# Optimization experiments

Measured on AMD Instinct MI355X. Metric: run time of the kernel, lower is better.

Reference implementation:

```python
import jax, jax.numpy as jnp
import numpy as np

DIM = 1536; NH = 12; HD = 128; C2 = HD // 2          # rope half-dim = 64
F, H, W = 1, 30, 52
FRAME = H * W                                         # 1560 tokens/frame
SINK_FRAMES = 1; LOCAL_ATTN = 6
SINK = SINK_FRAMES * FRAME                            # 1560
MAX_ATTN = LOCAL_ATTN * 1560                          # 9360
CACHE = 9360                                          # kv cache length
GLOBAL_END = 9360; LOCAL_END_CACHE = 9360             # cache state before step
SPLITS = (C2 - 2 * (C2 // 3), C2 // 3, C2 // 3)       # (22, 21, 21)
EPS = 1e-6


def setup_inputs() -> dict:
    key = jax.random.key(0)
    ks = jax.random.split(key, 12)
    s = F * H * W
    rn = lambda k, sh, sc=1.0: jax.random.normal(k, sh, jnp.float32) * sc
    x = rn(ks[0], (1, s, DIM))
    Wq = rn(ks[1], (DIM, DIM), 0.02); Wk = rn(ks[2], (DIM, DIM), 0.02)
    Wv = rn(ks[3], (DIM, DIM), 0.02); Wo = rn(ks[4], (DIM, DIM), 0.02)
    zb = jnp.zeros((DIM,), jnp.float32)
    angles = jax.random.uniform(ks[5], (1024, C2), jnp.float32) * (2.0 * np.pi)
    freqs_cos = jnp.cos(angles); freqs_sin = jnp.sin(angles)
    cache_k = rn(ks[6], (1, CACHE, NH, HD)); cache_v = rn(ks[7], (1, CACHE, NH, HD))
    return dict(x=x, Wq=Wq, bq=zb, Wk=Wk, bk=zb, Wv=Wv, bv=zb, Wo=Wo, bo=zb,
                nq_w=jnp.ones((DIM,), jnp.float32), nk_w=jnp.ones((DIM,), jnp.float32),
                cache_k=cache_k, cache_v=cache_v,
                freqs_cos=freqs_cos, freqs_sin=freqs_sin,
                seq_lens=jnp.array([s], jnp.int32),
                grid_sizes=jnp.array([[F, H, W]], jnp.int32),
                current_start=GLOBAL_END)


def _rmsnorm(x, w):
    return x * jax.lax.rsqrt(jnp.mean(x * x, -1, keepdims=True) + EPS) * w


def _grid_table(table, start_frame):
    """table [1024, C2] -> per-token rope factors [S, 1, C2] over the (F,H,W) grid."""
    s0, s1, s2 = SPLITS
    tf, th, tw = table[:, :s0], table[:, s0:s0 + s1], table[:, s0 + s1:]
    fp = jnp.broadcast_to(tf[start_frame:start_frame + F][:, None, None, :], (F, H, W, s0))
    hp = jnp.broadcast_to(th[:H][None, :, None, :], (F, H, W, s1))
    wp = jnp.broadcast_to(tw[:W][None, None, :, :], (F, H, W, s2))
    return jnp.concatenate([fp, hp, wp], -1).reshape(F * H * W, 1, C2)


def _rope(x, cos, sin):
    # x: [b, s, n, d]; cos/sin: [s, 1, C2] (complex multiply in real arithmetic)
    b, s, n, d = x.shape
    xp = x.reshape(b, s, n, d // 2, 2)
    xr, xi = xp[..., 0], xp[..., 1]
    c, sn = cos[None], sin[None]                      # [1, s, 1, C2]
    out_r = xr * c - xi * sn
    out_i = xr * sn + xi * c
    return jnp.stack([out_r, out_i], -1).reshape(b, s, n, d)


def reference(x, Wq, bq, Wk, bk, Wv, bv, Wo, bo, nq_w, nk_w,
              cache_k, cache_v, freqs_cos, freqs_sin,
              seq_lens, grid_sizes, current_start):
    b, s = x.shape[:2]
    q = _rmsnorm(x @ Wq.T + bq, nq_w).reshape(b, s, NH, HD)
    k = _rmsnorm(x @ Wk.T + bk, nk_w).reshape(b, s, NH, HD)
    v = (x @ Wv.T + bv).reshape(b, s, NH, HD)

    start_frame = int(current_start) // FRAME
    cos = _grid_table(freqs_cos, start_frame)
    sin = _grid_table(freqs_sin, start_frame)
    rq = _rope(q, cos, sin)
    rk = _rope(k, cos, sin)

    # --- static cache bookkeeping (roll_and_insert path; all Python ints) ---
    num_new = s
    current_end = int(current_start) + num_new
    num_evicted = num_new + LOCAL_END_CACHE - CACHE           # 1560
    num_rolled = LOCAL_END_CACHE - num_evicted - SINK         # 6240
    local_end = LOCAL_END_CACHE + current_end - GLOBAL_END - num_evicted  # 9360
    local_start = local_end - num_new                         # 7800 == SINK + num_rolled
    temp_k = jnp.concatenate(
        [cache_k[:, :SINK], cache_k[:, SINK + num_evicted:SINK + num_evicted + num_rolled], rk], axis=1)
    temp_v = jnp.concatenate(
        [cache_v[:, :SINK], cache_v[:, SINK + num_evicted:SINK + num_evicted + num_rolled], v], axis=1)

    # --- sink + sliding-window attention ---
    local_budget = MAX_ATTN - SINK
    win_start = max(SINK, local_end - local_budget)
    k_cat = jnp.concatenate([temp_k[:, :SINK], temp_k[:, win_start:local_end]], axis=1)
    v_cat = jnp.concatenate([temp_v[:, :SINK], temp_v[:, win_start:local_end]], axis=1)

    logits = jnp.einsum('bqhd,bkhd->bhqk', rq, k_cat) * (HD ** -0.5)
    probs = jax.nn.softmax(logits, axis=-1)
    out = jnp.einsum('bhqk,bkhd->bqhd', probs, v_cat)
    y = out.reshape(b, s, DIM) @ Wo.T + bo
    return y
```

## Files before the change

kernel.cpp:

```cpp
#include <hip/hip_runtime.h>
#include <hip/hip_bf16.h>

typedef __bf16 bf16;
typedef __bf16 bf16x2 __attribute__((ext_vector_type(2)));
typedef __bf16 bf16x4 __attribute__((ext_vector_type(4)));
typedef __bf16 bf16x8 __attribute__((ext_vector_type(8)));
typedef float f32x4 __attribute__((ext_vector_type(4)));
typedef float f32x16 __attribute__((ext_vector_type(16)));
typedef unsigned u32x2 __attribute__((ext_vector_type(2)));

#define DIM 1536
#define NH 12
#define HD 128
#define SEQ 1560
#define KV 9360
#define KVP 9408
#define SINK 1560
#define NEWBASE 7800
#define QSCALE_L2E (0.08838834764831845f * 1.4426950408889634f)
#define NSPLIT 3
#define CHUNK 3136
#define NT 98
#define KB 32
#define QBLK 128
#define NQT 13

__device__ __forceinline__ void gl_lds16(const void* g, void* l) {
  __builtin_amdgcn_global_load_lds(
      (const __attribute__((address_space(1))) unsigned int*)g,
      (__attribute__((address_space(3))) unsigned int*)l, 16, 0, 0);
}

__device__ __forceinline__ f32x16 mfma32(bf16x8 a, bf16x8 b, f32x16 c) {
  return __builtin_amdgcn_mfma_f32_32x32x16_bf16(a, b, c, 0, 0, 0);
}

struct CastBatch {
  const float* src[5];
  bf16* dst[5];
  int n[5];
};
__global__ __launch_bounds__(256) void castall(CastBatch cb) {
  const float* src = cb.src[blockIdx.y];
  bf16* dst = cb.dst[blockIdx.y];
  int n = cb.n[blockIdx.y];
  int i = (blockIdx.x * 256 + threadIdx.x) * 8;
  if (i < n) {
    float4 a = *(const float4*)(src + i);
    float4 b = *(const float4*)(src + i + 4);
    bf16x8 o;
    o[0] = (bf16)a.x; o[1] = (bf16)a.y; o[2] = (bf16)a.z; o[3] = (bf16)a.w;
    o[4] = (bf16)b.x; o[5] = (bf16)b.y; o[6] = (bf16)b.z; o[7] = (bf16)b.w;
    *(bf16x8*)(dst + i) = o;
  }
}

__global__ __launch_bounds__(256) void clear_pad(bf16* __restrict__ Kcat,
                                                 bf16* __restrict__ Vt) {
  int h = blockIdx.y;
  int i = blockIdx.x * 256 + threadIdx.x;
  if (i < (KVP - KV) * HD) {
    int r = KV + i / HD, d = i % HD;
    Kcat[((size_t)h * KVP + r) * HD + d] = (bf16)0.f;
    int dv = i / (KVP - KV), j = KV + i % (KVP - KV);
    Vt[((size_t)h * HD + dv) * KVP + j] = (bf16)0.f;
  }
}

struct GemmBatch {
  const bf16* B[3];
  const float* bias[3];
  float* C[3];
};

#define BM 128
#define BN 128
#define BK 32

__global__ __launch_bounds__(256, 2) void gemm_bt(const bf16* __restrict__ A,
                                                  GemmBatch gb, int M) {
  const bf16* Bw = gb.B[blockIdx.z];
  const float* bias = gb.bias[blockIdx.z];
  float* C = gb.C[blockIdx.z];
  int bm = blockIdx.x * BM;
  int bn = blockIdx.y * BN;

  __shared__ bf16 Alds[2][BM][BK];
  __shared__ bf16 Blds[2][BN][BK];

  int t = threadIdx.x;
  int lane = t & 63;
  int wave = t >> 6;
  int wr = wave >> 1, wc = wave & 1;
  int fr = lane & 15;
  int fo = (lane >> 4) * 8;

  f32x4 acc[4][4] = {};

  const int NK = DIM / BK;
  int colA = (lane & 3) * 8;
  int lrow = lane >> 2;

#define STAGEG(buf, k0)                                                     \
  {                                                                         \
    _Pragma("unroll") for (int p = 0; p < 2; ++p) {                         \
      int rbase = wave * 16 + p * 64;                                       \
      int ga = bm + rbase + lrow;                                           \
      if (ga > M - 1) ga = M - 1;                                           \
      gl_lds16(A + (size_t)ga * DIM + (k0) + colA, &Alds[buf][rbase][0]);   \
      int gbv = bn + rbase + lrow;                                          \
      gl_lds16(Bw + (size_t)gbv * DIM + (k0) + colA, &Blds[buf][rbase][0]); \
    }                                                                       \
  }

  STAGEG(0, 0);
  int cur = 0;
  for (int ks = 0; ks < NK; ++ks) {
    __syncthreads();
    if (ks + 1 < NK) STAGEG(cur ^ 1, (ks + 1) * BK);
    bf16x8 af[4], bfv[4];
#pragma unroll
    for (int i = 0; i < 4; ++i)
      af[i] = *(const bf16x8*)&Alds[cur][wr * 64 + i * 16 + fr][fo];
#pragma unroll
    for (int j = 0; j < 4; ++j)
      bfv[j] = *(const bf16x8*)&Blds[cur][wc * 64 + j * 16 + fr][fo];
#pragma unroll
    for (int i = 0; i < 4; ++i)
#pragma unroll
      for (int j = 0; j < 4; ++j)
        acc[i][j] = __builtin_amdgcn_mfma_f32_16x16x32_bf16(af[i], bfv[j],
                                                            acc[i][j], 0, 0, 0);
    cur ^= 1;
  }
#undef STAGEG

  int g4 = (lane >> 4) * 4;
#pragma unroll
  for (int i = 0; i < 4; ++i) {
    int mbase = bm + wr * 64 + i * 16 + g4;
#pragma unroll
    for (int j = 0; j < 4; ++j) {
      int col = bn + wc * 64 + j * 16 + fr;
      float bv = bias[col];
#pragma unroll
      for (int r = 0; r < 4; ++r) {
        int m = mbase + r;
        if (m < M) C[(size_t)m * DIM + col] = acc[i][j][r] + bv;
      }
    }
  }
}

__global__ __launch_bounds__(256) void norm_rope(
    const float* __restrict__ qraw, const float* __restrict__ kraw,
    const float* __restrict__ nqw, const float* __restrict__ nkw,
    const float* __restrict__ fcos, const float* __restrict__ fsin,
    bf16* __restrict__ Qh, bf16* __restrict__ Kcat) {
  int tok = blockIdx.x;
  int tid = threadIdx.x;
  const float* qr = qraw + (size_t)tok * DIM;
  const float* kr = kraw + (size_t)tok * DIM;
  float sq = 0.f, sk = 0.f;
  for (int c = tid; c < DIM; c += 256) {
    float a = qr[c];
    sq += a * a;
    float b = kr[c];
    sk += b * b;
  }
#pragma unroll
  for (int off = 32; off; off >>= 1) {
    sq += __shfl_down(sq, off);
    sk += __shfl_down(sk, off);
  }
  __shared__ float red[2][4];
  int w = tid >> 6;
  if ((tid & 63) == 0) {
    red[0][w] = sq;
    red[1][w] = sk;
  }
  __syncthreads();
  sq = red[0][0] + red[0][1] + red[0][2] + red[0][3];
  sk = red[1][0] + red[1][1] + red[1][2] + red[1][3];
  float rsq = rsqrtf(sq * (1.0f / DIM) + 1e-6f);
  float rsk = rsqrtf(sk * (1.0f / DIM) + 1e-6f);

  int hrow = tok / 52, wrow = tok % 52;
  for (int p = tid; p < NH * 64; p += 256) {
    int n = p >> 6, i = p & 63;
    int trow = (i < 22) ? 6 : (i < 43 ? hrow : wrow);
    float cs = fcos[trow * 64 + i];
    float sn = fsin[trow * 64 + i];
    int c = n * HD + 2 * i;
    float xr = qr[c] * rsq * nqw[c];
    float xi = qr[c + 1] * rsq * nqw[c + 1];
    bf16x2 qo;
    qo[0] = (bf16)((xr * cs - xi * sn) * QSCALE_L2E);
    qo[1] = (bf16)((xr * sn + xi * cs) * QSCALE_L2E);
    *(bf16x2*)(Qh + ((size_t)n * SEQ + tok) * HD + 2 * i) = qo;
    float yr = kr[c] * rsk * nkw[c];
    float yi = kr[c + 1] * rsk * nkw[c + 1];
    bf16x2 ko;
    ko[0] = (bf16)(yr * cs - yi * sn);
    ko[1] = (bf16)(yr * sn + yi * cs);
    *(bf16x2*)(Kcat + ((size_t)n * KVP + NEWBASE + tok) * HD + 2 * i) = ko;
  }
}

__global__ __launch_bounds__(256) void build_kcat(const float* __restrict__ cache_k,
                                                  bf16* __restrict__ Kcat) {
  int j = blockIdx.x;
  int src = j < SINK ? j : j + SINK;
  const float* sp = cache_k + (size_t)src * DIM;
  for (int c4 = threadIdx.x; c4 < DIM / 4; c4 += 256) {
    float4 v = *(const float4*)(sp + c4 * 4);
    int c = c4 * 4;
    int n = c >> 7, d = c & 127;
    bf16x4 o;
    o[0] = (bf16)v.x; o[1] = (bf16)v.y; o[2] = (bf16)v.z; o[3] = (bf16)v.w;
    *(bf16x4*)(Kcat + ((size_t)n * KVP + j) * HD + d) = o;
  }
}

__global__ __launch_bounds__(256) void build_vt(const float* __restrict__ cache_v,
                                                const float* __restrict__ vraw,
                                                bf16* __restrict__ Vt) {
  int h = blockIdx.y;
  int j0 = blockIdx.x * 64;
  __shared__ bf16 T[128][72];
  int tid = threadIdx.x;
  for (int idx = tid; idx < 64 * 32; idx += 256) {
    int jl = idx >> 5, s = idx & 31;
    int j = j0 + jl;
    if (j >= KV) continue;
    const float* sp;
    if (j < NEWBASE) {
      int srcj = j < SINK ? j : j + SINK;
      sp = cache_v + (size_t)srcj * DIM + h * HD;
    } else {
      sp = vraw + (size_t)(j - NEWBASE) * DIM + h * HD;
    }
    float4 v = *(const float4*)(sp + s * 4);
    T[s * 4 + 0][jl] = (bf16)v.x;
    T[s * 4 + 1][jl] = (bf16)v.y;
    T[s * 4 + 2][jl] = (bf16)v.z;
    T[s * 4 + 3][jl] = (bf16)v.w;
  }
  __syncthreads();
  for (int idx = tid; idx < 128 * 16; idx += 256) {
    int d = idx >> 4, g = idx & 15;
    int j = j0 + g * 4;
    if (j + 4 > KV) continue;
    bf16x4 o;
    o[0] = T[d][4 * g];
    o[1] = T[d][4 * g + 1];
    o[2] = T[d][4 * g + 2];
    o[3] = T[d][4 * g + 3];
    *(bf16x4*)(Vt + ((size_t)h * HD + d) * KVP + j) = o;
  }
}

__global__ __launch_bounds__(256, 2) void attn_split(const bf16* __restrict__ Qh,
                                                     const bf16* __restrict__ Kcat,
                                                     const bf16* __restrict__ Vtg,
                                                     float* __restrict__ Opart,
                                                     float* __restrict__ MLpart) {
  int orig = blockIdx.x;
  int xcd = orig & 7, jj = orig >> 3;
  int wgid = (xcd < 4 ? xcd * 59 : 236 + (xcd - 4) * 58) + jj;
  int qt = wgid % NQT;
  int h = (wgid / NQT) % NH;
  int sp = wgid / (NQT * NH);
  int q0 = qt * QBLK;
  int c0 = sp * CHUNK;

  int t = threadIdx.x, lane = t & 63, w = t >> 6;
  int ql = lane & 31, hi = lane >> 5;

  __shared__ __align__(16) bf16 Vlds[2][128 * KB];

  int qrow = q0 + w * 32 + ql;
  int qcl = qrow < SEQ ? qrow : SEQ - 1;
  const bf16* Qp = Qh + ((size_t)h * SEQ + qcl) * HD + hi * 8;
  bf16x8 qreg[8];
#pragma unroll
  for (int ks = 0; ks < 8; ++ks) qreg[ks] = *(const bf16x8*)(Qp + ks * 16);

  int vadd[2];
#pragma unroll
  for (int p = 0; p < 2; ++p) {
    int m = (2 * w + p) * 64 + lane;
    int dV = m >> 2, cV = m & 3;
    vadd[p] = dV * KVP + (cV ^ ((dV >> 1) & 3)) * 8;
  }

  int voff[4][2];
#pragma unroll
  for (int db = 0; db < 4; ++db)
#pragma unroll
    for (int ks = 0; ks < 2; ++ks)
      voff[db][ks] = (db * 32 + ql) * 64 + (((ks * 2 + hi) ^ ((ql >> 1) & 3)) * 16);

  const bf16* Vhp = Vtg + (size_t)h * HD * KVP;
  const bf16* Kl0 = Kcat + (size_t)h * KVP * HD + (size_t)(c0 + ql) * HD + hi * 8;

  f32x16 oacc[4] = {};
  float m_q = -1e38f, l_q = 0.f;

#define STAGEV(buf, j0v)                                                      \
  {                                                                           \
    const bf16* Vs = Vhp + (j0v);                                             \
    _Pragma("unroll") for (int p = 0; p < 2; ++p)                             \
        gl_lds16(Vs + vadd[p], (char*)&Vlds[buf][0] + w * 2048 + p * 1024);   \
  }

#define KLOAD(KR, TI)                                                         \
  {                                                                           \
    const bf16* Kl = Kl0 + (TI) * (KB * HD);                                  \
    _Pragma("unroll") for (int ks = 0; ks < 8; ++ks)                          \
        KR[ks] = *(const bf16x8*)(Kl + ks * 16);                              \
  }

#define TILE_BODY(KR, TI)                                                     \
  {                                                                           \
    int j0 = c0 + (TI)*KB;                                                    \
    const char* Vc = (const char*)&Vlds[cur][0];                              \
    f32x16 s0 = {};                                                           \
    __builtin_amdgcn_s_setprio(1);                                            \
    _Pragma("unroll") for (int ks = 0; ks < 8; ++ks)                          \
        s0 = mfma32(KR[ks], qreg[ks], s0);                                    \
    __builtin_amdgcn_s_setprio(0);                                            \
    if (j0 + KB > KV) {                                                       \
      _Pragma("unroll") for (int reg = 0; reg < 16; ++reg) {                  \
        int kk = (reg & 3) + 8 * (reg >> 2) + 4 * hi;                         \
        if (j0 + kk >= KV) s0[reg] = -1e38f;                                  \
      }                                                                       \
    }                                                                         \
    float m8[8];                                                              \
    _Pragma("unroll") for (int r = 0; r < 8; ++r)                             \
        m8[r] = fmaxf(s0[r], s0[r + 8]);                                      \
    float mx = fmaxf(fmaxf(fmaxf(m8[0], m8[4]), fmaxf(m8[1], m8[5])),         \
                     fmaxf(fmaxf(m8[2], m8[6]), fmaxf(m8[3], m8[7])));        \
    mx = fmaxf(mx, __shfl_xor(mx, 32));                                       \
    if (__any(mx - m_q > 8.f)) {                                              \
      float mnew = fmaxf(m_q, mx);                                            \
      float corr = exp2f(m_q - mnew);                                         \
      m_q = mnew;                                                             \
      l_q *= corr;                                                            \
      _Pragma("unroll") for (int reg = 0; reg < 16; ++reg) {                  \
        int qsrc = (reg & 3) + 8 * (reg >> 2) + 4 * hi;                       \
        float c = __shfl(corr, qsrc);                                         \
        _Pragma("unroll") for (int db = 0; db < 4; ++db) oacc[db][reg] *= c;  \
      }                                                                       \
    }                                                                         \
    _Pragma("unroll") for (int r = 0; r < 16; ++r)                            \
        s0[r] = exp2f(s0[r] - m_q);                                           \
    float t8[8];                                                              \
    _Pragma("unroll") for (int r = 0; r < 8; ++r) t8[r] = s0[r] + s0[r + 8];  \
    float sum = ((t8[0] + t8[4]) + (t8[1] + t8[5])) +                         \
                ((t8[2] + t8[6]) + (t8[3] + t8[7]));                          \
    sum += __shfl_xor(sum, 32);                                               \
    l_q += sum;                                                               \
    bf16x8 pa[2];                                                             \
    _Pragma("unroll") for (int ks = 0; ks < 2; ++ks) {                        \
      const int r0 = ks * 8;                                                  \
      bf16x2 p0, p1, p2, p3;                                                  \
      p0[0] = (bf16)s0[r0 + 0]; p0[1] = (bf16)s0[r0 + 1];                     \
      p1[0] = (bf16)s0[r0 + 2]; p1[1] = (bf16)s0[r0 + 3];                     \
      p2[0] = (bf16)s0[r0 + 4]; p2[1] = (bf16)s0[r0 + 5];                     \
      p3[0] = (bf16)s0[r0 + 6]; p3[1] = (bf16)s0[r0 + 7];                     \
      unsigned x0 = __builtin_bit_cast(unsigned, p0);                         \
      unsigned x1 = __builtin_bit_cast(unsigned, p1);                         \
      unsigned y0 = __builtin_bit_cast(unsigned, p2);                         \
      unsigned y1 = __builtin_bit_cast(unsigned, p3);                         \
      u32x2 r0v = __builtin_amdgcn_permlane32_swap(x0, y0, false, false);     \
      u32x2 r1v = __builtin_amdgcn_permlane32_swap(x1, y1, false, false);     \
      int4 tmp;                                                               \
      tmp.x = (int)r0v[0];                                                    \
      tmp.y = (int)r1v[0];                                                    \
      tmp.z = (int)r0v[1];                                                    \
      tmp.w = (int)r1v[1];                                                    \
      pa[ks] = __builtin_bit_cast(bf16x8, tmp);                               \
    }                                                                         \
    __builtin_amdgcn_s_setprio(1);                                            \
    _Pragma("unroll") for (int db = 0; db < 4; ++db)                          \
        _Pragma("unroll") for (int ks = 0; ks < 2; ++ks)                      \
            oacc[db] = mfma32(pa[ks], *(const bf16x8*)(Vc + voff[db][ks]),    \
                              oacc[db]);                                      \
    __builtin_amdgcn_s_setprio(0);                                            \
    __syncthreads();                                                          \
    cur ^= 1;                                                                 \
  }

  bf16x8 kA[8], kB[8];
  STAGEV(0, c0);
  KLOAD(kA, 0);
  __syncthreads();
  int cur = 0;

#pragma unroll 1
  for (int it = 0; it < NT / 2; ++it) {
    int ti = 2 * it;
    STAGEV(cur ^ 1, c0 + (ti + 1) * KB);
    KLOAD(kB, ti + 1);
    TILE_BODY(kA, ti);
    if (ti + 2 < NT) {
      STAGEV(cur ^ 1, c0 + (ti + 2) * KB);
      KLOAD(kA, ti + 2);
    }
    TILE_BODY(kB, ti + 1);
  }
#undef TILE_BODY
#undef KLOAD
#undef STAGEV

  float* Oh = Opart + ((size_t)sp * NH + h) * SEQ * HD;
  float* MLh = MLpart + ((size_t)sp * NH + h) * SEQ * 2;
#pragma unroll
  for (int reg = 0; reg < 16; ++reg) {
    int q = q0 + w * 32 + (reg & 3) + 8 * (reg >> 2) + 4 * hi;
    if (q >= SEQ) continue;
#pragma unroll
    for (int db = 0; db < 4; ++db)
      Oh[(size_t)q * HD + db * 32 + ql] = oacc[db][reg];
  }
  if (lane < 32) {
    int q = q0 + w * 32 + ql;
    if (q < SEQ) {
      MLh[q * 2 + 0] = m_q;
      MLh[q * 2 + 1] = l_q;
    }
  }
}

__global__ __launch_bounds__(256) void attn_merge(const float* __restrict__ Opart,
                                                  const float* __restrict__ MLpart,
                                                  bf16* __restrict__ Aout) {
  int idx = blockIdx.x * 2 + (threadIdx.x >> 7);
  if (idx >= NH * SEQ) return;
  int d = threadIdx.x & 127;
  int h = idx / SEQ, q = idx % SEQ;
  float m[NSPLIT];
  float M = -1e38f;
#pragma unroll
  for (int s = 0; s < NSPLIT; ++s) {
    m[s] = MLpart[(((size_t)s * NH + h) * SEQ + q) * 2];
    M = fmaxf(M, m[s]);
  }
  float L = 0.f, o = 0.f;
#pragma unroll
  for (int s = 0; s < NSPLIT; ++s) {
    float wgt = exp2f(m[s] - M);
    L += MLpart[(((size_t)s * NH + h) * SEQ + q) * 2 + 1] * wgt;
    o += Opart[((((size_t)s * NH + h) * SEQ + q)) * HD + d] * wgt;
  }
  Aout[(size_t)q * DIM + h * HD + d] = (bf16)(o / L);
}

extern "C" void kernel_launch(void* const* d_in, const int* in_sizes, int n_in,
                              void* d_out, int out_size, void* d_ws, size_t ws_size,
                              hipStream_t stream) {
  const float* x = (const float*)d_in[0];
  const float* Wq = (const float*)d_in[1];
  const float* bq = (const float*)d_in[2];
  const float* Wk = (const float*)d_in[3];
  const float* bk = (const float*)d_in[4];
  const float* Wv = (const float*)d_in[5];
  const float* bv = (const float*)d_in[6];
  const float* Wo = (const float*)d_in[7];
  const float* bo = (const float*)d_in[8];
  const float* nqw = (const float*)d_in[9];
  const float* nkw = (const float*)d_in[10];
  const float* cache_k = (const float*)d_in[11];
  const float* cache_v = (const float*)d_in[12];
  const float* fcos = (const float*)d_in[13];
  const float* fsin = (const float*)d_in[14];
  float* out = (float*)d_out;

  char* ws = (char*)d_ws;
  size_t off = 0;
  auto alloc = [&](size_t bytes) {
    char* p = ws + off;
    off += (bytes + 255) & ~(size_t)255;
    return p;
  };
  const int XN = SEQ * DIM;
  const int WN = DIM * DIM;
  bf16* xb = (bf16*)alloc((size_t)XN * 2);
  bf16* Wqb = (bf16*)alloc((size_t)WN * 2);
  bf16* Wkb = (bf16*)alloc((size_t)WN * 2);
  bf16* Wvb = (bf16*)alloc((size_t)WN * 2);
  bf16* Wob = (bf16*)alloc((size_t)WN * 2);
  bf16* QhB = (bf16*)alloc((size_t)NH * SEQ * HD * 2);
  bf16* Kcat = (bf16*)alloc((size_t)NH * KVP * HD * 2);
  bf16* Vt = (bf16*)alloc((size_t)NH * HD * KVP * 2);
  bf16* Aout = (bf16*)alloc((size_t)XN * 2);
  float* MLpart = (float*)alloc((size_t)NSPLIT * NH * SEQ * 2 * 4);
  float* Opart = (float*)alloc((size_t)NSPLIT * NH * SEQ * HD * 4);
  float* qraw = Opart;
  float* kraw = qraw + XN;
  float* vraw = kraw + XN;

  CastBatch cb;
  cb.src[0] = x;  cb.dst[0] = xb;  cb.n[0] = XN;
  cb.src[1] = Wq; cb.dst[1] = Wqb; cb.n[1] = WN;
  cb.src[2] = Wk; cb.dst[2] = Wkb; cb.n[2] = WN;
  cb.src[3] = Wv; cb.dst[3] = Wvb; cb.n[3] = WN;
  cb.src[4] = Wo; cb.dst[4] = Wob; cb.n[4] = WN;
  castall<<<dim3((XN + 2047) / 2048, 5), 256, 0, stream>>>(cb);

  clear_pad<<<dim3(((KVP - KV) * HD + 255) / 256, NH), 256, 0, stream>>>(Kcat, Vt);

  GemmBatch gqkv;
  gqkv.B[0] = Wqb; gqkv.B[1] = Wkb; gqkv.B[2] = Wvb;
  gqkv.bias[0] = bq; gqkv.bias[1] = bk; gqkv.bias[2] = bv;
  gqkv.C[0] = qraw; gqkv.C[1] = kraw; gqkv.C[2] = vraw;
  gemm_bt<<<dim3(13, 12, 3), 256, 0, stream>>>(xb, gqkv, SEQ);

  norm_rope<<<SEQ, 256, 0, stream>>>(qraw, kraw, nqw, nkw, fcos, fsin, QhB, Kcat);
  build_kcat<<<NEWBASE, 256, 0, stream>>>(cache_k, Kcat);
  build_vt<<<dim3(147, NH), 256, 0, stream>>>(cache_v, vraw, Vt);

  attn_split<<<dim3(NQT * NH * NSPLIT), 256, 0, stream>>>(QhB, Kcat, Vt, Opart, MLpart);
  attn_merge<<<(NH * SEQ + 1) / 2, 256, 0, stream>>>(Opart, MLpart, Aout);

  GemmBatch gout;
  gout.B[0] = Wob; gout.B[1] = Wob; gout.B[2] = Wob;
  gout.bias[0] = bo; gout.bias[1] = bo; gout.bias[2] = bo;
  gout.C[0] = out; gout.C[1] = out; gout.C[2] = out;
  gemm_bt<<<dim3(13, 12, 1), 256, 0, stream>>>(Aout, gout, SEQ);
}
```

Measured before the change: 352.2 us.

## Stage K through LDS and software-pipeline QK^T one tile ahead of softmax-PV

K tiles are now staged into swizzled LDS with async global-to-LDS copies, replacing direct per-lane register loads. V gets a triple buffer. The loop is restructured so QK^T for tile i runs alongside softmax and PV for tile i-1, letting the MFMA work of the two stages interleave with the exp/reduction work. This costs more LDS (two K buffers plus three V buffers per block) and extra LDS reads for K, which may reduce occupancy or add bank traffic.

```diff
diff --git a/kernel.cpp b/kernel.cpp
--- a/kernel.cpp
+++ b/kernel.cpp
@@ -277,7 +277,8 @@
   int t = threadIdx.x, lane = t & 63, w = t >> 6;
   int ql = lane & 31, hi = lane >> 5;
 
-  __shared__ __align__(16) bf16 Vlds[2][128 * KB];
+  __shared__ __align__(16) bf16 Klds[2][KB * 128];
+  __shared__ __align__(16) bf16 Vlds[3][128 * KB];
 
   int qrow = q0 + w * 32 + ql;
   int qcl = qrow < SEQ ? qrow : SEQ - 1;
@@ -286,14 +287,20 @@
 #pragma unroll
   for (int ks = 0; ks < 8; ++ks) qreg[ks] = *(const bf16x8*)(Qp + ks * 16);
 
-  int vadd[2];
+  int kadd[2], vadd[2];
 #pragma unroll
   for (int p = 0; p < 2; ++p) {
     int m = (2 * w + p) * 64 + lane;
+    int rK = m >> 4, cK = m & 15;
+    kadd[p] = rK * HD + (cK ^ (rK & 15)) * 8;
     int dV = m >> 2, cV = m & 3;
     vadd[p] = dV * KVP + (cV ^ ((dV >> 1) & 3)) * 8;
   }
 
+  int koff[8];
+#pragma unroll
+  for (int ks = 0; ks < 8; ++ks)
+    koff[ks] = ql * 256 + (((ks * 2 + hi) ^ (ql & 15)) * 16);
   int voff[4][2];
 #pragma unroll
   for (int db = 0; db < 4; ++db)
@@ -301,44 +308,52 @@
     for (int ks = 0; ks < 2; ++ks)
       voff[db][ks] = (db * 32 + ql) * 64 + (((ks * 2 + hi) ^ ((ql >> 1) & 3)) * 16);
 
+  const bf16* Khp = Kcat + (size_t)h * KVP * HD;
   const bf16* Vhp = Vtg + (size_t)h * HD * KVP;
-  const bf16* Kl0 = Kcat + (size_t)h * KVP * HD + (size_t)(c0 + ql) * HD + hi * 8;
+  char* Kb = (char*)&Klds[0][0];
+  char* Vb = (char*)&Vlds[0][0];
 
   f32x16 oacc[4] = {};
   float m_q = -1e38f, l_q = 0.f;
-
-#define STAGEV(buf, j0v)                                                      \
+  f32x16 sA, sB;
+  int vst, vpv;
+
+#define STAGEK(kbuf, TIs)                                                     \
   {                                                                           \
-    const bf16* Vs = Vhp + (j0v);                                             \
+    const bf16* Ks = Khp + (size_t)(c0 + (TIs)*KB) * HD;                      \
     _Pragma("unroll") for (int p = 0; p < 2; ++p)                             \
-        gl_lds16(Vs + vadd[p], (char*)&Vlds[buf][0] + w * 2048 + p * 1024);   \
-  }
-
-#define KLOAD(KR, TI)                                                         \
+        gl_lds16(Ks + kadd[p], Kb + (kbuf)*8192 + w * 2048 + p * 1024);       \
+  }
+#define STAGEV(vbuf, TIs)                                                     \
   {                                                                           \
-    const bf16* Kl = Kl0 + (TI) * (KB * HD);                                  \
-    _Pragma("unroll") for (int ks = 0; ks < 8; ++ks)                          \
-        KR[ks] = *(const bf16x8*)(Kl + ks * 16);                              \
-  }
-
-#define TILE_BODY(KR, TI)                                                     \
+    const bf16* Vs = Vhp + (c0 + (TIs)*KB);                                   \
+    _Pragma("unroll") for (int p = 0; p < 2; ++p)                             \
+        gl_lds16(Vs + vadd[p], Vb + (vbuf)*8192 + w * 2048 + p * 1024);       \
+  }
+
+#define QKT(SC, KQK, TI)                                                      \
   {                                                                           \
-    int j0 = c0 + (TI)*KB;                                                    \
-    const char* Vc = (const char*)&Vlds[cur][0];                              \
-    f32x16 s0 = {};                                                           \
+    const char* Kc = Kb + (KQK)*8192;                                         \
+    f32x16 stmp = {};                                                         \
     __builtin_amdgcn_s_setprio(1);                                            \
     _Pragma("unroll") for (int ks = 0; ks < 8; ++ks)                          \
-        s0 = mfma32(KR[ks], qreg[ks], s0);                                    \
+        stmp = mfma32(*(const bf16x8*)(Kc + koff[ks]), qreg[ks], stmp);       \
     __builtin_amdgcn_s_setprio(0);                                            \
-    if (j0 + KB > KV) {                                                       \
+    int j0m = c0 + (TI)*KB;                                                   \
+    if (j0m + KB > KV) {                                                      \
       _Pragma("unroll") for (int reg = 0; reg < 16; ++reg) {                  \
         int kk = (reg & 3) + 8 * (reg >> 2) + 4 * hi;                         \
-        if (j0 + kk >= KV) s0[reg] = -1e38f;                                  \
+        if (j0m + kk >= KV) stmp[reg] = -1e38f;                               \
       }                                                                       \
     }                                                                         \
+    SC = stmp;                                                                \
+  }
+
+#define SMPV(SP)                                                              \
+  {                                                                           \
     float m8[8];                                                              \
     _Pragma("unroll") for (int r = 0; r < 8; ++r)                             \
-        m8[r] = fmaxf(s0[r], s0[r + 8]);                                      \
+        m8[r] = fmaxf(SP[r], SP[r + 8]);                                      \
     float mx = fmaxf(fmaxf(fmaxf(m8[0], m8[4]), fmaxf(m8[1], m8[5])),         \
                      fmaxf(fmaxf(m8[2], m8[6]), fmaxf(m8[3], m8[7])));        \
     mx = fmaxf(mx, __shfl_xor(mx, 32));                                       \
@@ -354,9 +369,9 @@
       }                                                                       \
     }                                                                         \
     _Pragma("unroll") for (int r = 0; r < 16; ++r)                            \
-        s0[r] = exp2f(s0[r] - m_q);                                           \
+        SP[r] = exp2f(SP[r] - m_q);                                           \
     float t8[8];                                                              \
-    _Pragma("unroll") for (int r = 0; r < 8; ++r) t8[r] = s0[r] + s0[r + 8];  \
+    _Pragma("unroll") for (int r = 0; r < 8; ++r) t8[r] = SP[r] + SP[r + 8];  \
     float sum = ((t8[0] + t8[4]) + (t8[1] + t8[5])) +                         \
                 ((t8[2] + t8[6]) + (t8[3] + t8[7]));                          \
     sum += __shfl_xor(sum, 32);                                               \
@@ -365,10 +380,10 @@
     _Pragma("unroll") for (int ks = 0; ks < 2; ++ks) {                        \
       const int r0 = ks * 8;                                                  \
       bf16x2 p0, p1, p2, p3;                                                  \
-      p0[0] = (bf16)s0[r0 + 0]; p0[1] = (bf16)s0[r0 + 1];                     \
-      p1[0] = (bf16)s0[r0 + 2]; p1[1] = (bf16)s0[r0 + 3];                     \
-      p2[0] = (bf16)s0[r0 + 4]; p2[1] = (bf16)s0[r0 + 5];                     \
-      p3[0] = (bf16)s0[r0 + 6]; p3[1] = (bf16)s0[r0 + 7];                     \
+      p0[0] = (bf16)SP[r0 + 0]; p0[1] = (bf16)SP[r0 + 1];                     \
+      p1[0] = (bf16)SP[r0 + 2]; p1[1] = (bf16)SP[r0 + 3];                     \
+      p2[0] = (bf16)SP[r0 + 4]; p2[1] = (bf16)SP[r0 + 5];                     \
+      p3[0] = (bf16)SP[r0 + 6]; p3[1] = (bf16)SP[r0 + 7];                     \
       unsigned x0 = __builtin_bit_cast(unsigned, p0);                         \
       unsigned x1 = __builtin_bit_cast(unsigned, p1);                         \
       unsigned y0 = __builtin_bit_cast(unsigned, p2);                         \
@@ -382,37 +397,50 @@
       tmp.w = (int)r1v[1];                                                    \
       pa[ks] = __builtin_bit_cast(bf16x8, tmp);                               \
     }                                                                         \
+    const char* Vc = Vb + vpv * 8192;                                         \
     __builtin_amdgcn_s_setprio(1);                                            \
     _Pragma("unroll") for (int db = 0; db < 4; ++db)                          \
         _Pragma("unroll") for (int ks = 0; ks < 2; ++ks)                      \
             oacc[db] = mfma32(pa[ks], *(const bf16x8*)(Vc + voff[db][ks]),    \
                               oacc[db]);                                      \
     __builtin_amdgcn_s_setprio(0);                                            \
+  }
+
+#define BODY(TI, SC, SP, KQK, KST)                                            \
+  {                                                                           \
+    if ((TI) + 1 < NT) {                                                      \
+      STAGEK(KST, (TI) + 1);                                                  \
+      STAGEV(vst, (TI) + 1);                                                  \
+    }                                                                         \
+    QKT(SC, KQK, TI);                                                         \
+    SMPV(SP);                                                                 \
     __syncthreads();                                                          \
-    cur ^= 1;                                                                 \
-  }
-
-  bf16x8 kA[8], kB[8];
-  STAGEV(0, c0);
-  KLOAD(kA, 0);
+    vst = vst == 2 ? 0 : vst + 1;                                             \
+    vpv = vpv == 2 ? 0 : vpv + 1;                                             \
+  }
+
+  STAGEK(0, 0);
+  STAGEV(0, 0);
   __syncthreads();
-  int cur = 0;
-
+  STAGEK(1, 1);
+  STAGEV(1, 1);
+  QKT(sA, 0, 0);
+  __syncthreads();
+  vst = 2;
+  vpv = 0;
+  BODY(1, sB, sA, 1, 0);
 #pragma unroll 1
-  for (int it = 0; it < NT / 2; ++it) {
-    int ti = 2 * it;
-    STAGEV(cur ^ 1, c0 + (ti + 1) * KB);
-    KLOAD(kB, ti + 1);
-    TILE_BODY(kA, ti);
-    if (ti + 2 < NT) {
-      STAGEV(cur ^ 1, c0 + (ti + 2) * KB);
-      KLOAD(kA, ti + 2);
-    }
-    TILE_BODY(kB, ti + 1);
-  }
-#undef TILE_BODY
-#undef KLOAD
+  for (int it = 0; it < 48; ++it) {
+    int ti = 2 + 2 * it;
+    BODY(ti, sA, sB, 0, 1);
+    BODY(ti + 1, sB, sA, 1, 0);
+  }
+  SMPV(sB);
+#undef BODY
+#undef SMPV
+#undef QKT
 #undef STAGEV
+#undef STAGEK
 
   float* Oh = Opart + ((size_t)sp * NH + h) * SEQ * HD;
   float* MLh = MLpart + ((size_t)sp * NH + h) * SEQ * 2;
```

Measured after the change: 303.2 us. 1.16x faster.
